# Kernel optimization log

Measured on AMD Instinct MI355X. Metric: run time of the kernel, lower is better.

The kernel has to match this reference:

```python
import jax, jax.numpy as jnp
import numpy as np

MSA_DIM = 256
N_HEADS = 8
HEAD_DIM = MSA_DIM // N_HEADS
PAIR_DIM = 128
SCALE = 1.0 / float(np.sqrt(HEAD_DIM))


def setup_inputs() -> dict:
    key = jax.random.key(0)
    ks = jax.random.split(key, 7)
    B, S, L = 1, 128, 384
    return {
        "msa": jax.random.normal(ks[0], (B, S, L, MSA_DIM), dtype=jnp.float32),
        "pair": jax.random.normal(ks[1], (B, L, L, PAIR_DIM), dtype=jnp.float32),
        "Wq": jax.random.normal(ks[2], (MSA_DIM, MSA_DIM), dtype=jnp.float32) * 0.02,
        "Wk": jax.random.normal(ks[3], (MSA_DIM, MSA_DIM), dtype=jnp.float32) * 0.02,
        "Wv": jax.random.normal(ks[4], (MSA_DIM, MSA_DIM), dtype=jnp.float32) * 0.02,
        "Wo": jax.random.normal(ks[5], (MSA_DIM, MSA_DIM), dtype=jnp.float32) * 0.02,
        "Wpb": jax.random.normal(ks[6], (N_HEADS, PAIR_DIM), dtype=jnp.float32) * 0.02,
    }


def reference(msa, pair, Wq, Wk, Wv, Wo, Wpb):
    B, S, L, D = msa.shape
    H, hd = N_HEADS, HEAD_DIM
    # projections (nn.Linear: y = x @ W.T), split heads -> (B,S,H,L,hd)
    q = (msa @ Wq.T).reshape(B, S, L, H, hd)
    k = (msa @ Wk.T).reshape(B, S, L, H, hd)
    v = (msa @ Wv.T).reshape(B, S, L, H, hd)
    # NOTE: faithful to the original forward — pair_bias is computed but the
    # Triton kernel performs plain flash attention, so the bias is NOT added.
    _pair_bias = jnp.einsum('bijp,hp->bhij', pair, Wpb)  # dead code, as in source
    # attention logits per MSA row: (B,S,H,L,L)
    scores = jnp.einsum('bslhd,bsmhd->bshlm', q, k) * SCALE
    attn = jax.nn.softmax(scores, axis=-1)
    out = jnp.einsum('bshlm,bsmhd->bslhd', attn, v).reshape(B, S, L, D)
    return out @ Wo.T
```

## Files before the change

### kernel.cpp

```cpp
#include <hip/hip_runtime.h>
#include <stdint.h>

typedef unsigned short u16;
typedef __bf16 bf16x8 __attribute__((ext_vector_type(8)));
typedef float f32x4 __attribute__((ext_vector_type(4)));

#define NROWS    49152
#define MSA_N    12582912
#define QKV_OFF  12582912

__device__ __forceinline__ u16 f2bf(float x) {
    unsigned int u = __float_as_uint(x);
    u += 0x7fffu + ((u >> 16) & 1u);
    return (u16)(u >> 16);
}
__device__ __forceinline__ float bf2f(u16 h) {
    return __uint_as_float(((unsigned int)h) << 16);
}

__global__ void convert_msa(const float* __restrict__ src, u16* __restrict__ dst) {
    int i = blockIdx.x * 256 + threadIdx.x;
    float4 v = ((const float4*)src)[i];
    ushort4 o;
    o.x = f2bf(v.x); o.y = f2bf(v.y); o.z = f2bf(v.z); o.w = f2bf(v.w);
    ((ushort4*)dst)[i] = o;
}

__global__ void pack_weights(const float* __restrict__ Wq, const float* __restrict__ Wk,
                             const float* __restrict__ Wv, const float* __restrict__ Wo,
                             u16* __restrict__ Wqkv, u16* __restrict__ Woh, u16* __restrict__ Wol) {
    int i = blockIdx.x * 256 + threadIdx.x;
    Wqkv[i]           = f2bf(Wq[i]);
    Wqkv[65536 + i]   = f2bf(Wk[i]);
    Wqkv[131072 + i]  = f2bf(Wv[i]);
    float w = Wo[i];
    u16 hi = f2bf(w);
    Woh[i] = hi;
    Wol[i] = f2bf(w - bf2f(hi));
}

__launch_bounds__(256, 2)
__global__ void qkv_gemm(const u16* __restrict__ A, const u16* __restrict__ W,
                         u16* __restrict__ Qkv) {
    __shared__ __align__(16) u16 As[128 * 32];
    __shared__ __align__(16) u16 Bs[128 * 32];
    const int tid = threadIdx.x;
    const int tm = blockIdx.x % 384, tn = blockIdx.x / 384;
    const int lane = tid & 63, wave = tid >> 6;
    const int lm = lane & 15, lq = lane >> 4;
    const int wm = (wave >> 1) * 64, wn = (wave & 1) * 64;
    f32x4 acc[4][4] = {};

    const int ra = tid >> 2, ka = (tid & 3) << 3;
    const int rb = (tid + 256) >> 2;

    for (int k0 = 0; k0 < 256; k0 += 32) {
        *(uint4*)&As[ra * 32 + ka] = *(const uint4*)&A[(tm * 128 + ra) * 256 + k0 + ka];
        *(uint4*)&As[rb * 32 + ka] = *(const uint4*)&A[(tm * 128 + rb) * 256 + k0 + ka];
        *(uint4*)&Bs[ra * 32 + ka] = *(const uint4*)&W[(tn * 128 + ra) * 256 + k0 + ka];
        *(uint4*)&Bs[rb * 32 + ka] = *(const uint4*)&W[(tn * 128 + rb) * 256 + k0 + ka];
        __syncthreads();
        bf16x8 af[4], bfr[4];
        #pragma unroll
        for (int i = 0; i < 4; ++i)
            af[i] = *(const bf16x8*)&As[(wm + i * 16 + lm) * 32 + lq * 8];
        #pragma unroll
        for (int j = 0; j < 4; ++j)
            bfr[j] = *(const bf16x8*)&Bs[(wn + j * 16 + lm) * 32 + lq * 8];
        #pragma unroll
        for (int i = 0; i < 4; ++i)
            #pragma unroll
            for (int j = 0; j < 4; ++j)
                acc[i][j] = __builtin_amdgcn_mfma_f32_16x16x32_bf16(af[i], bfr[j], acc[i][j], 0, 0, 0);
        __syncthreads();
    }
    #pragma unroll
    for (int i = 0; i < 4; ++i) {
        #pragma unroll
        for (int j = 0; j < 4; ++j) {
            #pragma unroll
            for (int r = 0; r < 4; ++r) {
                int R = tm * 128 + wm + i * 16 + lq * 4 + r;
                int C = tn * 128 + wn + j * 16 + lm;
                int s = R / 384, l = R - s * 384;
                int which = C >> 8, h = (C >> 5) & 7, d = C & 31;
                Qkv[which * QKV_OFF + (((s << 3) + h) * 384 + l) * 32 + d] = f2bf(acc[i][j][r]);
            }
        }
    }
}

__launch_bounds__(256, 2)
__global__ void msa_attention(const u16* __restrict__ Qkv,
                              u16* __restrict__ Ahi, u16* __restrict__ Alo) {
    __shared__ __align__(16) u16 Ks[384 * 32];
    __shared__ __align__(16) u16 Vt[31 * 392 + 384];
    __shared__ __align__(16) u16 Ps[4][572];
    const int tid = threadIdx.x;
    const int sh = blockIdx.x;
    const int s = sh >> 3, h = sh & 7;
    const u16* Qg = Qkv + (size_t)sh * 12288;
    const u16* Kg = Qg + QKV_OFF;
    const u16* Vg = Qg + 2 * QKV_OFF;

    for (int i = tid; i < 1536; i += 256)
        *(uint4*)&Ks[i * 8] = *(const uint4*)&Kg[i * 8];
    for (int i = tid; i < 1536; i += 256) {
        int m = i >> 2, d0 = (i & 3) << 3;
        uint4 v = *(const uint4*)&Vg[i * 8];
        unsigned int p[4] = {v.x, v.y, v.z, v.w};
        #pragma unroll
        for (int jj = 0; jj < 4; ++jj) {
            Vt[(d0 + 2 * jj) * 392 + m]     = (u16)(p[jj] & 0xffffu);
            Vt[(d0 + 2 * jj + 1) * 392 + m] = (u16)(p[jj] >> 16);
        }
    }
    __syncthreads();

    const int lane = tid & 63, wave = tid >> 6;
    const int lm = lane & 15, lq = lane >> 4;
    const float CEXP = 0.17677669529663687f * 1.4426950408889634f;
    u16* pw = &Ps[wave][0];

    union Frag { bf16x8 v; struct { uint2 a, b; } u; };

    for (int it = 0; it < 6; ++it) {
        const int l0 = (it * 4 + wave) * 16;
        bf16x8 aq = *(const bf16x8*)&Qg[(l0 + lm) * 32 + lq * 8];
        f32x4 o0 = {}, o1 = {};
        float ls[4] = {0.f, 0.f, 0.f, 0.f};
        for (int n0 = 0; n0 < 384; n0 += 32) {
            bf16x8 bk0 = *(const bf16x8*)&Ks[(n0 + lm) * 32 + lq * 8];
            bf16x8 bk1 = *(const bf16x8*)&Ks[(n0 + 16 + lm) * 32 + lq * 8];
            f32x4 z = {};
            f32x4 s0 = __builtin_amdgcn_mfma_f32_16x16x32_bf16(aq, bk0, z, 0, 0, 0);
            f32x4 s1 = __builtin_amdgcn_mfma_f32_16x16x32_bf16(aq, bk1, z, 0, 0, 0);
            #pragma unroll
            for (int r = 0; r < 4; ++r) {
                float p0 = exp2f(s0[r] * CEXP);
                float p1 = exp2f(s1[r] * CEXP);
                ls[r] += p0 + p1;
                pw[(lq * 4 + r) * 36 + lm]      = f2bf(p0);
                pw[(lq * 4 + r) * 36 + 16 + lm] = f2bf(p1);
            }
            asm volatile("s_waitcnt lgkmcnt(0)" ::: "memory");
            Frag ap;
            ap.u.a = *(const uint2*)&pw[lm * 36 + lq * 8];
            ap.u.b = *(const uint2*)&pw[lm * 36 + lq * 8 + 4];
            bf16x8 bv0 = *(const bf16x8*)&Vt[lm * 392 + n0 + lq * 8];
            bf16x8 bv1 = *(const bf16x8*)&Vt[(16 + lm) * 392 + n0 + lq * 8];
            o0 = __builtin_amdgcn_mfma_f32_16x16x32_bf16(ap.v, bv0, o0, 0, 0, 0);
            o1 = __builtin_amdgcn_mfma_f32_16x16x32_bf16(ap.v, bv1, o1, 0, 0, 0);
        }
        #pragma unroll
        for (int r = 0; r < 4; ++r) {
            float L = ls[r];
            L += __shfl_xor(L, 1);
            L += __shfl_xor(L, 2);
            L += __shfl_xor(L, 4);
            L += __shfl_xor(L, 8);
            float inv = 1.0f / L;
            float x0 = o0[r] * inv, x1 = o1[r] * inv;
            int Arow = s * 384 + l0 + lq * 4 + r;
            int c0 = h * 32 + lm, c1 = c0 + 16;
            u16 h0 = f2bf(x0), h1 = f2bf(x1);
            Ahi[Arow * 256 + c0] = h0;
            Alo[Arow * 256 + c0] = f2bf(x0 - bf2f(h0));
            Ahi[Arow * 256 + c1] = h1;
            Alo[Arow * 256 + c1] = f2bf(x1 - bf2f(h1));
        }
    }
}

__launch_bounds__(256, 2)
__global__ void out_gemm(const u16* __restrict__ Ahi, const u16* __restrict__ Alo,
                         const u16* __restrict__ Woh, const u16* __restrict__ Wol,
                         float* __restrict__ out) {
    __shared__ __align__(16) u16 Ah[128 * 32], Al[128 * 32], Bh[128 * 32], Bl[128 * 32];
    const int tid = threadIdx.x;
    const int tm = blockIdx.x % 384, tn = blockIdx.x / 384;
    const int lane = tid & 63, wave = tid >> 6;
    const int lm = lane & 15, lq = lane >> 4;
    const int wm = (wave >> 1) * 64, wn = (wave & 1) * 64;
    f32x4 acc[4][4] = {};

    const int ra = tid >> 2, ka = (tid & 3) << 3;
    const int rb = (tid + 256) >> 2;

    for (int k0 = 0; k0 < 256; k0 += 32) {
        *(uint4*)&Ah[ra * 32 + ka] = *(const uint4*)&Ahi[(tm * 128 + ra) * 256 + k0 + ka];
        *(uint4*)&Ah[rb * 32 + ka] = *(const uint4*)&Ahi[(tm * 128 + rb) * 256 + k0 + ka];
        *(uint4*)&Al[ra * 32 + ka] = *(const uint4*)&Alo[(tm * 128 + ra) * 256 + k0 + ka];
        *(uint4*)&Al[rb * 32 + ka] = *(const uint4*)&Alo[(tm * 128 + rb) * 256 + k0 + ka];
        *(uint4*)&Bh[ra * 32 + ka] = *(const uint4*)&Woh[(tn * 128 + ra) * 256 + k0 + ka];
        *(uint4*)&Bh[rb * 32 + ka] = *(const uint4*)&Woh[(tn * 128 + rb) * 256 + k0 + ka];
        *(uint4*)&Bl[ra * 32 + ka] = *(const uint4*)&Wol[(tn * 128 + ra) * 256 + k0 + ka];
        *(uint4*)&Bl[rb * 32 + ka] = *(const uint4*)&Wol[(tn * 128 + rb) * 256 + k0 + ka];
        __syncthreads();
        bf16x8 ahf[4], alf[4], bhf[4], blf[4];
        #pragma unroll
        for (int i = 0; i < 4; ++i) {
            ahf[i] = *(const bf16x8*)&Ah[(wm + i * 16 + lm) * 32 + lq * 8];
            alf[i] = *(const bf16x8*)&Al[(wm + i * 16 + lm) * 32 + lq * 8];
        }
        #pragma unroll
        for (int j = 0; j < 4; ++j) {
            bhf[j] = *(const bf16x8*)&Bh[(wn + j * 16 + lm) * 32 + lq * 8];
            blf[j] = *(const bf16x8*)&Bl[(wn + j * 16 + lm) * 32 + lq * 8];
        }
        #pragma unroll
        for (int i = 0; i < 4; ++i)
            #pragma unroll
            for (int j = 0; j < 4; ++j) {
                acc[i][j] = __builtin_amdgcn_mfma_f32_16x16x32_bf16(alf[i], bhf[j], acc[i][j], 0, 0, 0);
                acc[i][j] = __builtin_amdgcn_mfma_f32_16x16x32_bf16(ahf[i], blf[j], acc[i][j], 0, 0, 0);
                acc[i][j] = __builtin_amdgcn_mfma_f32_16x16x32_bf16(ahf[i], bhf[j], acc[i][j], 0, 0, 0);
            }
        __syncthreads();
    }
    #pragma unroll
    for (int i = 0; i < 4; ++i)
        #pragma unroll
        for (int j = 0; j < 4; ++j)
            #pragma unroll
            for (int r = 0; r < 4; ++r) {
                int R = tm * 128 + wm + i * 16 + lq * 4 + r;
                int C = tn * 128 + wn + j * 16 + lm;
                out[R * 256 + C] = acc[i][j][r];
            }
}

extern "C" void kernel_launch(void* const* d_in, const int* in_sizes, int n_in,
                              void* d_out, int out_size, void* d_ws, size_t ws_size,
                              hipStream_t stream) {
    const float* msa = (const float*)d_in[0];
    const float* Wq = (const float*)d_in[2];
    const float* Wk = (const float*)d_in[3];
    const float* Wv = (const float*)d_in[4];
    const float* Wo = (const float*)d_in[5];
    char* ws = (char*)d_ws;
    u16* msa_bf = (u16*)(ws + 0);
    u16* Qkv    = (u16*)(ws + 25165824);
    u16* Ahi    = (u16*)(ws + 100663296);
    u16* Alo    = (u16*)(ws + 125829120);
    u16* Wqkv   = (u16*)(ws + 150994944);
    u16* Woh    = (u16*)(ws + 151388160);
    u16* Wol    = (u16*)(ws + 151519232);
    float* out  = (float*)d_out;

    hipLaunchKernelGGL(convert_msa, dim3(12288), dim3(256), 0, stream, msa, msa_bf);
    hipLaunchKernelGGL(pack_weights, dim3(256), dim3(256), 0, stream, Wq, Wk, Wv, Wo, Wqkv, Woh, Wol);
    hipLaunchKernelGGL(qkv_gemm, dim3(2304), dim3(256), 0, stream, msa_bf, Wqkv, Qkv);
    hipLaunchKernelGGL(msa_attention, dim3(1024), dim3(256), 0, stream, Qkv, Ahi, Alo);
    hipLaunchKernelGGL(out_gemm, dim3(768), dim3(256), 0, stream, Ahi, Alo, Woh, Wol, out);
}
```

Baseline: 293.0 us.

## Emit transposed V from QKV GEMM and keep softmax probabilities in registers

The QKV GEMM swaps its operand roles for Q/K tiles so each lane writes 4 contiguous elements, folds the softmax scale into Q, and writes V already transposed. This removes the scalar LDS transpose in the attention kernel. Attention now computes S^T so the probabilities land directly in the 16x16x16 MFMA operand layout, removing the LDS round trip for P. It also processes all six query tiles per K/V chunk with Q held in registers, and uses a hardware exp2 and reciprocal. The output GEMM is transposed the same way to allow vector float4 stores. The costs are higher register pressure from 12 accumulators and reliance on the _1k MFMA builtin.

After: 283.6 us. 1.03x faster.

```diff
diff --git a/kernel.cpp b/kernel.cpp
--- a/kernel.cpp
+++ b/kernel.cpp
@@ -3,11 +3,10 @@
 
 typedef unsigned short u16;
 typedef __bf16 bf16x8 __attribute__((ext_vector_type(8)));
+typedef short s16x4 __attribute__((ext_vector_type(4)));
 typedef float f32x4 __attribute__((ext_vector_type(4)));
 
-#define NROWS    49152
-#define MSA_N    12582912
-#define QKV_OFF  12582912
+#define QKV_STRIDE 12288
 
 __device__ __forceinline__ u16 f2bf(float x) {
     unsigned int u = __float_as_uint(x);
@@ -16,6 +15,21 @@
 }
 __device__ __forceinline__ float bf2f(u16 h) {
     return __uint_as_float(((unsigned int)h) << 16);
+}
+__device__ __forceinline__ float tbf(float x) {
+    return __uint_as_float(__float_as_uint(x) & 0xffff0000u);
+}
+
+static __device__ __forceinline__ f32x4 pv_mfma(s16x4 a, s16x4 b, f32x4 c) {
+#if __has_builtin(__builtin_amdgcn_mfma_f32_16x16x16bf16_1k)
+    return __builtin_amdgcn_mfma_f32_16x16x16bf16_1k(a, b, c, 0, 0, 0);
+#else
+    union { s16x4 h[2]; bf16x8 v; } ua, ub;
+    s16x4 zz = {0, 0, 0, 0};
+    ua.h[0] = a; ua.h[1] = zz;
+    ub.h[0] = b; ub.h[1] = zz;
+    return __builtin_amdgcn_mfma_f32_16x16x32_bf16(ua.v, ub.v, c, 0, 0, 0);
+#endif
 }
 
 __global__ void convert_msa(const float* __restrict__ src, u16* __restrict__ dst) {
@@ -30,9 +44,9 @@
                              const float* __restrict__ Wv, const float* __restrict__ Wo,
                              u16* __restrict__ Wqkv, u16* __restrict__ Woh, u16* __restrict__ Wol) {
     int i = blockIdx.x * 256 + threadIdx.x;
-    Wqkv[i]           = f2bf(Wq[i]);
-    Wqkv[65536 + i]   = f2bf(Wk[i]);
-    Wqkv[131072 + i]  = f2bf(Wv[i]);
+    Wqkv[i]          = f2bf(Wq[i]);
+    Wqkv[65536 + i]  = f2bf(Wk[i]);
+    Wqkv[131072 + i] = f2bf(Wv[i]);
     float w = Wo[i];
     u16 hi = f2bf(w);
     Woh[i] = hi;
@@ -41,18 +55,20 @@
 
 __launch_bounds__(256, 2)
 __global__ void qkv_gemm(const u16* __restrict__ A, const u16* __restrict__ W,
-                         u16* __restrict__ Qkv) {
+                         u16* __restrict__ Qb, u16* __restrict__ Kb, u16* __restrict__ VTb) {
     __shared__ __align__(16) u16 As[128 * 32];
     __shared__ __align__(16) u16 Bs[128 * 32];
     const int tid = threadIdx.x;
     const int tm = blockIdx.x % 384, tn = blockIdx.x / 384;
+    const bool trans = (tn < 4);
     const int lane = tid & 63, wave = tid >> 6;
     const int lm = lane & 15, lq = lane >> 4;
     const int wm = (wave >> 1) * 64, wn = (wave & 1) * 64;
+    const float CEXPF = 0.17677669529663687f * 1.4426950408889634f;
     f32x4 acc[4][4] = {};
 
     const int ra = tid >> 2, ka = (tid & 3) << 3;
-    const int rb = (tid + 256) >> 2;
+    const int rb = ra + 64;
 
     for (int k0 = 0; k0 < 256; k0 += 32) {
         *(uint4*)&As[ra * 32 + ka] = *(const uint4*)&A[(tm * 128 + ra) * 256 + k0 + ka];
@@ -60,114 +76,147 @@
         *(uint4*)&Bs[ra * 32 + ka] = *(const uint4*)&W[(tn * 128 + ra) * 256 + k0 + ka];
         *(uint4*)&Bs[rb * 32 + ka] = *(const uint4*)&W[(tn * 128 + rb) * 256 + k0 + ka];
         __syncthreads();
-        bf16x8 af[4], bfr[4];
+        const u16* Xs = trans ? Bs : As;
+        const u16* Ys = trans ? As : Bs;
+        bf16x8 xf[4], yf[4];
         #pragma unroll
         for (int i = 0; i < 4; ++i)
-            af[i] = *(const bf16x8*)&As[(wm + i * 16 + lm) * 32 + lq * 8];
+            xf[i] = *(const bf16x8*)&Xs[(wm + i * 16 + lm) * 32 + lq * 8];
         #pragma unroll
         for (int j = 0; j < 4; ++j)
-            bfr[j] = *(const bf16x8*)&Bs[(wn + j * 16 + lm) * 32 + lq * 8];
+            yf[j] = *(const bf16x8*)&Ys[(wn + j * 16 + lm) * 32 + lq * 8];
         #pragma unroll
         for (int i = 0; i < 4; ++i)
             #pragma unroll
             for (int j = 0; j < 4; ++j)
-                acc[i][j] = __builtin_amdgcn_mfma_f32_16x16x32_bf16(af[i], bfr[j], acc[i][j], 0, 0, 0);
+                acc[i][j] = __builtin_amdgcn_mfma_f32_16x16x32_bf16(xf[i], yf[j], acc[i][j], 0, 0, 0);
         __syncthreads();
     }
-    #pragma unroll
-    for (int i = 0; i < 4; ++i) {
+
+    if (trans) {
+        #pragma unroll
+        for (int i = 0; i < 4; ++i) {
+            int F0 = tn * 128 + wm + i * 16 + lq * 4;
+            int which = F0 >> 8;
+            int h = (F0 >> 5) & 7, d0 = F0 & 31;
+            u16* dst = which ? Kb : Qb;
+            float scale = which ? 1.0f : CEXPF;
+            #pragma unroll
+            for (int j = 0; j < 4; ++j) {
+                int R = tm * 128 + wn + j * 16 + lm;
+                int s = R / 384, l = R - s * 384;
+                ushort4 o;
+                o.x = f2bf(acc[i][j][0] * scale);
+                o.y = f2bf(acc[i][j][1] * scale);
+                o.z = f2bf(acc[i][j][2] * scale);
+                o.w = f2bf(acc[i][j][3] * scale);
+                *(ushort4*)&dst[((s * 8 + h) * 384 + l) * 32 + d0] = o;
+            }
+        }
+    } else {
         #pragma unroll
         for (int j = 0; j < 4; ++j) {
-            #pragma unroll
-            for (int r = 0; r < 4; ++r) {
-                int R = tm * 128 + wm + i * 16 + lq * 4 + r;
-                int C = tn * 128 + wn + j * 16 + lm;
-                int s = R / 384, l = R - s * 384;
-                int which = C >> 8, h = (C >> 5) & 7, d = C & 31;
-                Qkv[which * QKV_OFF + (((s << 3) + h) * 384 + l) * 32 + d] = f2bf(acc[i][j][r]);
+            int F = tn * 128 + wn + j * 16 + lm;
+            int h = (F >> 5) & 7, d = F & 31;
+            #pragma unroll
+            for (int i = 0; i < 4; ++i) {
+                int R0 = tm * 128 + wm + i * 16 + lq * 4;
+                int s = R0 / 384, l0 = R0 - s * 384;
+                ushort4 o;
+                o.x = f2bf(acc[i][j][0]);
+                o.y = f2bf(acc[i][j][1]);
+                o.z = f2bf(acc[i][j][2]);
+                o.w = f2bf(acc[i][j][3]);
+                *(ushort4*)&VTb[((s * 8 + h) * 32 + d) * 384 + l0] = o;
             }
         }
     }
 }
 
-__launch_bounds__(256, 2)
-__global__ void msa_attention(const u16* __restrict__ Qkv,
+__launch_bounds__(256, 3)
+__global__ void msa_attention(const u16* __restrict__ Qb, const u16* __restrict__ Kb,
+                              const u16* __restrict__ VTb,
                               u16* __restrict__ Ahi, u16* __restrict__ Alo) {
     __shared__ __align__(16) u16 Ks[384 * 32];
-    __shared__ __align__(16) u16 Vt[31 * 392 + 384];
-    __shared__ __align__(16) u16 Ps[4][572];
+    __shared__ __align__(16) u16 Vt[32 * 392];
     const int tid = threadIdx.x;
     const int sh = blockIdx.x;
     const int s = sh >> 3, h = sh & 7;
-    const u16* Qg = Qkv + (size_t)sh * 12288;
-    const u16* Kg = Qg + QKV_OFF;
-    const u16* Vg = Qg + 2 * QKV_OFF;
+    const u16* Qg = Qb + (size_t)sh * QKV_STRIDE;
+    const u16* Kg = Kb + (size_t)sh * QKV_STRIDE;
+    const u16* Vg = VTb + (size_t)sh * QKV_STRIDE;
 
     for (int i = tid; i < 1536; i += 256)
         *(uint4*)&Ks[i * 8] = *(const uint4*)&Kg[i * 8];
     for (int i = tid; i < 1536; i += 256) {
-        int m = i >> 2, d0 = (i & 3) << 3;
-        uint4 v = *(const uint4*)&Vg[i * 8];
-        unsigned int p[4] = {v.x, v.y, v.z, v.w};
-        #pragma unroll
-        for (int jj = 0; jj < 4; ++jj) {
-            Vt[(d0 + 2 * jj) * 392 + m]     = (u16)(p[jj] & 0xffffu);
-            Vt[(d0 + 2 * jj + 1) * 392 + m] = (u16)(p[jj] >> 16);
-        }
-    }
-    __syncthreads();
+        int d = i / 48, c = i - d * 48;
+        *(uint4*)&Vt[d * 392 + c * 8] = *(const uint4*)&Vg[d * 384 + c * 8];
+    }
 
     const int lane = tid & 63, wave = tid >> 6;
     const int lm = lane & 15, lq = lane >> 4;
-    const float CEXP = 0.17677669529663687f * 1.4426950408889634f;
-    u16* pw = &Ps[wave][0];
-
-    union Frag { bf16x8 v; struct { uint2 a, b; } u; };
-
+
+    bf16x8 aq[6];
+    #pragma unroll
+    for (int it = 0; it < 6; ++it)
+        aq[it] = *(const bf16x8*)&Qg[((it * 4 + wave) * 16 + lm) * 32 + lq * 8];
+    __syncthreads();
+
+    f32x4 o[6][2] = {};
+    float ls[6] = {0.f, 0.f, 0.f, 0.f, 0.f, 0.f};
+
+    for (int n0 = 0; n0 < 384; n0 += 32) {
+        bf16x8 kf0 = *(const bf16x8*)&Ks[(n0 + lm) * 32 + lq * 8];
+        bf16x8 kf1 = *(const bf16x8*)&Ks[(n0 + 16 + lm) * 32 + lq * 8];
+        s16x4 vf00 = *(const s16x4*)&Vt[lm * 392 + n0 + lq * 4];
+        s16x4 vf01 = *(const s16x4*)&Vt[lm * 392 + n0 + 16 + lq * 4];
+        s16x4 vf10 = *(const s16x4*)&Vt[(16 + lm) * 392 + n0 + lq * 4];
+        s16x4 vf11 = *(const s16x4*)&Vt[(16 + lm) * 392 + n0 + 16 + lq * 4];
+        #pragma unroll
+        for (int it = 0; it < 6; ++it) {
+            f32x4 z = {0.f, 0.f, 0.f, 0.f};
+            f32x4 s0 = __builtin_amdgcn_mfma_f32_16x16x32_bf16(kf0, aq[it], z, 0, 0, 0);
+            f32x4 s1 = __builtin_amdgcn_mfma_f32_16x16x32_bf16(kf1, aq[it], z, 0, 0, 0);
+            float p0[4], p1[4];
+            float a = 0.f;
+            #pragma unroll
+            for (int r = 0; r < 4; ++r) {
+                p0[r] = __builtin_amdgcn_exp2f(s0[r]);
+                p1[r] = __builtin_amdgcn_exp2f(s1[r]);
+                a += tbf(p0[r]) + tbf(p1[r]);
+            }
+            ls[it] += a;
+            union { s16x4 v; uint2 u; } pk0, pk1;
+            pk0.u.x = __builtin_amdgcn_perm(__float_as_uint(p0[1]), __float_as_uint(p0[0]), 0x07060302u);
+            pk0.u.y = __builtin_amdgcn_perm(__float_as_uint(p0[3]), __float_as_uint(p0[2]), 0x07060302u);
+            pk1.u.x = __builtin_amdgcn_perm(__float_as_uint(p1[1]), __float_as_uint(p1[0]), 0x07060302u);
+            pk1.u.y = __builtin_amdgcn_perm(__float_as_uint(p1[3]), __float_as_uint(p1[2]), 0x07060302u);
+            o[it][0] = pv_mfma(vf00, pk0.v, o[it][0]);
+            o[it][0] = pv_mfma(vf01, pk1.v, o[it][0]);
+            o[it][1] = pv_mfma(vf10, pk0.v, o[it][1]);
+            o[it][1] = pv_mfma(vf11, pk1.v, o[it][1]);
+        }
+    }
+
+    #pragma unroll
     for (int it = 0; it < 6; ++it) {
-        const int l0 = (it * 4 + wave) * 16;
-        bf16x8 aq = *(const bf16x8*)&Qg[(l0 + lm) * 32 + lq * 8];
-        f32x4 o0 = {}, o1 = {};
-        float ls[4] = {0.f, 0.f, 0.f, 0.f};
-        for (int n0 = 0; n0 < 384; n0 += 32) {
-            bf16x8 bk0 = *(const bf16x8*)&Ks[(n0 + lm) * 32 + lq * 8];
-            bf16x8 bk1 = *(const bf16x8*)&Ks[(n0 + 16 + lm) * 32 + lq * 8];
-            f32x4 z = {};
-            f32x4 s0 = __builtin_amdgcn_mfma_f32_16x16x32_bf16(aq, bk0, z, 0, 0, 0);
-            f32x4 s1 = __builtin_amdgcn_mfma_f32_16x16x32_bf16(aq, bk1, z, 0, 0, 0);
-            #pragma unroll
-            for (int r = 0; r < 4; ++r) {
-                float p0 = exp2f(s0[r] * CEXP);
-                float p1 = exp2f(s1[r] * CEXP);
-                ls[r] += p0 + p1;
-                pw[(lq * 4 + r) * 36 + lm]      = f2bf(p0);
-                pw[(lq * 4 + r) * 36 + 16 + lm] = f2bf(p1);
-            }
-            asm volatile("s_waitcnt lgkmcnt(0)" ::: "memory");
-            Frag ap;
-            ap.u.a = *(const uint2*)&pw[lm * 36 + lq * 8];
-            ap.u.b = *(const uint2*)&pw[lm * 36 + lq * 8 + 4];
-            bf16x8 bv0 = *(const bf16x8*)&Vt[lm * 392 + n0 + lq * 8];
-            bf16x8 bv1 = *(const bf16x8*)&Vt[(16 + lm) * 392 + n0 + lq * 8];
-            o0 = __builtin_amdgcn_mfma_f32_16x16x32_bf16(ap.v, bv0, o0, 0, 0, 0);
-            o1 = __builtin_amdgcn_mfma_f32_16x16x32_bf16(ap.v, bv1, o1, 0, 0, 0);
-        }
-        #pragma unroll
-        for (int r = 0; r < 4; ++r) {
-            float L = ls[r];
-            L += __shfl_xor(L, 1);
-            L += __shfl_xor(L, 2);
-            L += __shfl_xor(L, 4);
-            L += __shfl_xor(L, 8);
-            float inv = 1.0f / L;
-            float x0 = o0[r] * inv, x1 = o1[r] * inv;
-            int Arow = s * 384 + l0 + lq * 4 + r;
-            int c0 = h * 32 + lm, c1 = c0 + 16;
-            u16 h0 = f2bf(x0), h1 = f2bf(x1);
-            Ahi[Arow * 256 + c0] = h0;
-            Alo[Arow * 256 + c0] = f2bf(x0 - bf2f(h0));
-            Ahi[Arow * 256 + c1] = h1;
-            Alo[Arow * 256 + c1] = f2bf(x1 - bf2f(h1));
+        float L = ls[it];
+        L += __shfl_xor(L, 16, 64);
+        L += __shfl_xor(L, 32, 64);
+        float inv = __builtin_amdgcn_rcpf(L);
+        int l = (it * 4 + wave) * 16 + lm;
+        int base = (s * 384 + l) * 256 + h * 32 + lq * 4;
+        #pragma unroll
+        for (int dt = 0; dt < 2; ++dt) {
+            ushort4 oh, ol;
+            float x0 = o[it][dt][0] * inv, x1 = o[it][dt][1] * inv;
+            float x2 = o[it][dt][2] * inv, x3 = o[it][dt][3] * inv;
+            oh.x = f2bf(x0); ol.x = f2bf(x0 - bf2f(oh.x));
+            oh.y = f2bf(x1); ol.y = f2bf(x1 - bf2f(oh.y));
+            oh.z = f2bf(x2); ol.z = f2bf(x2 - bf2f(oh.z));
+            oh.w = f2bf(x3); ol.w = f2bf(x3 - bf2f(oh.w));
+            *(ushort4*)&Ahi[base + dt * 16] = oh;
+            *(ushort4*)&Alo[base + dt * 16] = ol;
         }
     }
 }
@@ -185,7 +234,7 @@
     f32x4 acc[4][4] = {};
 
     const int ra = tid >> 2, ka = (tid & 3) << 3;
-    const int rb = (tid + 256) >> 2;
+    const int rb = ra + 64;
 
     for (int k0 = 0; k0 < 256; k0 += 32) {
         *(uint4*)&Ah[ra * 32 + ka] = *(const uint4*)&Ahi[(tm * 128 + ra) * 256 + k0 + ka];
@@ -197,37 +246,36 @@
         *(uint4*)&Bl[ra * 32 + ka] = *(const uint4*)&Wol[(tn * 128 + ra) * 256 + k0 + ka];
         *(uint4*)&Bl[rb * 32 + ka] = *(const uint4*)&Wol[(tn * 128 + rb) * 256 + k0 + ka];
         __syncthreads();
-        bf16x8 ahf[4], alf[4], bhf[4], blf[4];
+        bf16x8 whf[4], wlf[4], ahf[4], alf[4];
         #pragma unroll
         for (int i = 0; i < 4; ++i) {
-            ahf[i] = *(const bf16x8*)&Ah[(wm + i * 16 + lm) * 32 + lq * 8];
-            alf[i] = *(const bf16x8*)&Al[(wm + i * 16 + lm) * 32 + lq * 8];
+            whf[i] = *(const bf16x8*)&Bh[(wm + i * 16 + lm) * 32 + lq * 8];
+            wlf[i] = *(const bf16x8*)&Bl[(wm + i * 16 + lm) * 32 + lq * 8];
         }
         #pragma unroll
         for (int j = 0; j < 4; ++j) {
-            bhf[j] = *(const bf16x8*)&Bh[(wn + j * 16 + lm) * 32 + lq * 8];
-            blf[j] = *(const bf16x8*)&Bl[(wn + j * 16 + lm) * 32 + lq * 8];
+            ahf[j] = *(const bf16x8*)&Ah[(wn + j * 16 + lm) * 32 + lq * 8];
+            alf[j] = *(const bf16x8*)&Al[(wn + j * 16 + lm) * 32 + lq * 8];
         }
         #pragma unroll
         for (int i = 0; i < 4; ++i)
             #pragma unroll
             for (int j = 0; j < 4; ++j) {
-                acc[i][j] = __builtin_amdgcn_mfma_f32_16x16x32_bf16(alf[i], bhf[j], acc[i][j], 0, 0, 0);
-                acc[i][j] = __builtin_amdgcn_mfma_f32_16x16x32_bf16(ahf[i], blf[j], acc[i][j], 0, 0, 0);
-                acc[i][j] = __builtin_amdgcn_mfma_f32_16x16x32_bf16(ahf[i], bhf[j], acc[i][j], 0, 0, 0);
+                acc[i][j] = __builtin_amdgcn_mfma_f32_16x16x32_bf16(whf[i], alf[j], acc[i][j], 0, 0, 0);
+                acc[i][j] = __builtin_amdgcn_mfma_f32_16x16x32_bf16(wlf[i], ahf[j], acc[i][j], 0, 0, 0);
+                acc[i][j] = __builtin_amdgcn_mfma_f32_16x16x32_bf16(whf[i], ahf[j], acc[i][j], 0, 0, 0);
             }
         __syncthreads();
     }
     #pragma unroll
-    for (int i = 0; i < 4; ++i)
-        #pragma unroll
-        for (int j = 0; j < 4; ++j)
-            #pragma unroll
-            for (int r = 0; r < 4; ++r) {
-                int R = tm * 128 + wm + i * 16 + lq * 4 + r;
-                int C = tn * 128 + wn + j * 16 + lm;
-                out[R * 256 + C] = acc[i][j][r];
-            }
+    for (int i = 0; i < 4; ++i) {
+        int F0 = tn * 128 + wm + i * 16 + lq * 4;
+        #pragma unroll
+        for (int j = 0; j < 4; ++j) {
+            int R = tm * 128 + wn + j * 16 + lm;
+            *(f32x4*)&out[R * 256 + F0] = acc[i][j];
+        }
+    }
 }
 
 extern "C" void kernel_launch(void* const* d_in, const int* in_sizes, int n_in,
@@ -240,7 +288,9 @@
     const float* Wo = (const float*)d_in[5];
     char* ws = (char*)d_ws;
     u16* msa_bf = (u16*)(ws + 0);
-    u16* Qkv    = (u16*)(ws + 25165824);
+    u16* Qb     = (u16*)(ws + 25165824);
+    u16* Kb     = (u16*)(ws + 50331648);
+    u16* VTb    = (u16*)(ws + 75497472);
     u16* Ahi    = (u16*)(ws + 100663296);
     u16* Alo    = (u16*)(ws + 125829120);
     u16* Wqkv   = (u16*)(ws + 150994944);
@@ -250,7 +300,7 @@
 
     hipLaunchKernelGGL(convert_msa, dim3(12288), dim3(256), 0, stream, msa, msa_bf);
     hipLaunchKernelGGL(pack_weights, dim3(256), dim3(256), 0, stream, Wq, Wk, Wv, Wo, Wqkv, Woh, Wol);
-    hipLaunchKernelGGL(qkv_gemm, dim3(2304), dim3(256), 0, stream, msa_bf, Wqkv, Qkv);
-    hipLaunchKernelGGL(msa_attention, dim3(1024), dim3(256), 0, stream, Qkv, Ahi, Alo);
+    hipLaunchKernelGGL(qkv_gemm, dim3(2304), dim3(256), 0, stream, msa_bf, Wqkv, Qb, Kb, VTb);
+    hipLaunchKernelGGL(msa_attention, dim3(1024), dim3(256), 0, stream, Qb, Kb, VTb, Ahi, Alo);
     hipLaunchKernelGGL(out_gemm, dim3(768), dim3(256), 0, stream, Ahi, Alo, Woh, Wol, out);
 }
```
